# Optimization experiments

Measured on AMD Instinct MI355X. Metric: run time of the kernel, lower is better.

Reference implementation:

```python
import jax, jax.numpy as jnp
import numpy as np

EPS = 1e-12  # F.normalize eps
ALPHA = 1.0


def setup_inputs() -> dict:
    key = jax.random.key(0)
    k1, k2, k3, k4 = jax.random.split(key, 4)
    n_nodes, n_edges, d_in, d_out = 50000, 800000, 128, 128
    x = jax.random.normal(k1, (n_nodes, d_in), dtype=jnp.float32)
    W1 = jax.random.normal(k2, (d_out, d_in), dtype=jnp.float32) * (1.0 / np.sqrt(d_in))
    W2 = jax.random.normal(k3, (d_out, d_in), dtype=jnp.float32) * (1.0 / np.sqrt(d_in))
    edge_index = jax.random.randint(k4, (2, n_edges), 0, n_nodes, dtype=jnp.int64)
    return {"x": x, "W1": W1, "W2": W2, "edge_index": edge_index}


def reference(x, W1, W2, edge_index):
    n_nodes = x.shape[0]
    src, dst = edge_index[0], edge_index[1]
    # h_src = fc2(x)
    h = jnp.einsum('nd,od->no', x, W2)
    # out-degree normalization: h *= (deg_out + 1)^(-1/2)
    deg = jax.ops.segment_sum(jnp.ones(src.shape[0], dtype=x.dtype), src,
                              num_segments=n_nodes)
    h = h * ((deg + 1.0) ** -0.5)[:, None]
    # L2 normalize per node (F.normalize p=2 dim=1)
    nrm = jnp.sqrt(jnp.sum(h * h, axis=1, keepdims=True))
    h = h / jnp.maximum(nrm, EPS)
    # gather along edges, scatter-max to destinations
    msg = h[src]                                   # [E, d_out]
    agg = jax.ops.segment_max(msg, dst, num_segments=n_nodes)
    agg = jnp.where(jnp.isfinite(agg), agg, 0.0)   # empty segments -> 0 (torch_scatter semantics)
    # alpha * fc1(x) + aggregated messages
    return ALPHA * jnp.einsum('nd,od->no', x, W1) + agg
```

## Files before the change

### kernel.cpp

```cpp
#include <hip/hip_runtime.h>
#include <stdint.h>

#define N_NODES 50000
#define N_EDGES 800000
#define D 128
#define CAP 64
#define LDK 136

typedef __attribute__((ext_vector_type(8))) short short8;
typedef __attribute__((ext_vector_type(4))) float f32x4;
typedef __attribute__((ext_vector_type(4))) unsigned short ush4;

__device__ __forceinline__ unsigned short f2bf(float f) {
    uint32_t u = __float_as_uint(f);
    u += 0x7FFFu + ((u >> 16) & 1u);
    return (unsigned short)(u >> 16);
}
__device__ __forceinline__ float bflo(uint32_t u) { return __uint_as_float(u << 16); }
__device__ __forceinline__ float bfhi(uint32_t u) { return __uint_as_float(u & 0xFFFF0000u); }

__global__ __launch_bounds__(512) void gemm_fused(const float* __restrict__ x,
                                                  const float* __restrict__ W1,
                                                  const float* __restrict__ W2,
                                                  float* __restrict__ out,
                                                  unsigned short* __restrict__ hbf,
                                                  int* __restrict__ cnt)
{
    __shared__ unsigned short ws[256][LDK];
    __shared__ unsigned short xs[128][LDK];

    const int t    = threadIdx.x;
    const int row0 = blockIdx.x * 128;

    {
        int ci = blockIdx.x * 512 + t;
        if (ci < N_NODES) cnt[ci] = 0;
    }

    #pragma unroll
    for (int it = 0; it < 16; ++it) {
        int idx = it * 512 + t;
        int n = idx >> 5, c4 = idx & 31;
        const float* Wp = (n < 128) ? (W1 + (size_t)n * D) : (W2 + (size_t)(n - 128) * D);
        float4 v = *(const float4*)(Wp + c4 * 4);
        ush4 p; p[0] = f2bf(v.x); p[1] = f2bf(v.y); p[2] = f2bf(v.z); p[3] = f2bf(v.w);
        *(ush4*)&ws[n][c4 * 4] = p;
    }
    #pragma unroll
    for (int it = 0; it < 8; ++it) {
        int idx = it * 512 + t;
        int r = idx >> 5, c4 = idx & 31;
        int gr = row0 + r;
        float4 v = make_float4(0.f, 0.f, 0.f, 0.f);
        if (gr < N_NODES) v = *(const float4*)(x + (size_t)gr * D + c4 * 4);
        ush4 p; p[0] = f2bf(v.x); p[1] = f2bf(v.y); p[2] = f2bf(v.z); p[3] = f2bf(v.w);
        *(ush4*)&xs[r][c4 * 4] = p;
    }
    __syncthreads();

    const int wave = t >> 6;
    const int lane = t & 63;
    const int g    = lane >> 4;
    const int ln   = lane & 15;

    short8 afrag[4];
    #pragma unroll
    for (int ks = 0; ks < 4; ++ks)
        afrag[ks] = *(const short8*)&xs[wave * 16 + ln][ks * 32 + g * 8];

    f32x4 acc1[8], acc2[8];
    #pragma unroll
    for (int ct = 0; ct < 8; ++ct) {
        f32x4 a1 = {0.f, 0.f, 0.f, 0.f}, a2 = {0.f, 0.f, 0.f, 0.f};
        #pragma unroll
        for (int ks = 0; ks < 4; ++ks) {
            short8 b1 = *(const short8*)&ws[      ct * 16 + ln][ks * 32 + g * 8];
            short8 b2 = *(const short8*)&ws[128 + ct * 16 + ln][ks * 32 + g * 8];
            a1 = __builtin_amdgcn_mfma_f32_16x16x32_bf16(afrag[ks], b1, a1, 0, 0, 0);
            a2 = __builtin_amdgcn_mfma_f32_16x16x32_bf16(afrag[ks], b2, a2, 0, 0, 0);
        }
        acc1[ct] = a1; acc2[ct] = a2;
    }

    float ss[4] = {0.f, 0.f, 0.f, 0.f};
    #pragma unroll
    for (int ct = 0; ct < 8; ++ct)
        #pragma unroll
        for (int r = 0; r < 4; ++r)
            ss[r] = fmaf(acc2[ct][r], acc2[ct][r], ss[r]);
    #pragma unroll
    for (int r = 0; r < 4; ++r)
        #pragma unroll
        for (int o = 1; o < 16; o <<= 1)
            ss[r] += __shfl_xor(ss[r], o, 64);
    float scale[4];
    #pragma unroll
    for (int r = 0; r < 4; ++r)
        scale[r] = 1.0f / fmaxf(sqrtf(ss[r]), 1e-12f);

    #pragma unroll
    for (int r = 0; r < 4; ++r) {
        int grow = row0 + wave * 16 + g * 4 + r;
        if (grow < N_NODES) {
            #pragma unroll
            for (int ct = 0; ct < 8; ++ct) {
                out[(size_t)grow * D + ct * 16 + ln] = acc1[ct][r];
                hbf[(size_t)grow * D + ct * 16 + ln] = f2bf(acc2[ct][r] * scale[r]);
            }
        }
    }
}

__global__ __launch_bounds__(256) void fill_buckets(const int* __restrict__ ei,
                                                    int* __restrict__ cnt,
                                                    int* __restrict__ bucket)
{
    int i      = blockIdx.x * 256 + threadIdx.x;
    int stride = gridDim.x * 256;
    for (int e = i; e < N_EDGES; e += stride) {
        int s = ei[e];
        int d = ei[N_EDGES + e];
        int p = atomicAdd(&cnt[d], 1);
        if (p < CAP) bucket[d * CAP + p] = s;
    }
}

__global__ __launch_bounds__(256) void gather_max(const unsigned short* __restrict__ hbf,
                                                  const int* __restrict__ cnt,
                                                  const int* __restrict__ bucket,
                                                  float* __restrict__ out)
{
    int wid  = (blockIdx.x * 256 + threadIdx.x) >> 6;
    int lane = threadIdx.x & 63;
    if (wid >= N_NODES) return;
    int deg = cnt[wid];
    deg = (deg > CAP) ? CAP : deg;
    if (deg == 0) return;

    const uint32_t* h32 = (const uint32_t*)hbf;
    int sl = (lane < deg) ? bucket[wid * CAP + lane] : 0;

    float mx = -INFINITY, my = -INFINITY;
    int j = 0;
    for (; j + 4 <= deg; j += 4) {
        int s0 = __shfl(sl, j,     64);
        int s1 = __shfl(sl, j + 1, 64);
        int s2 = __shfl(sl, j + 2, 64);
        int s3 = __shfl(sl, j + 3, 64);
        uint32_t u0 = h32[(size_t)s0 * 64 + lane];
        uint32_t u1 = h32[(size_t)s1 * 64 + lane];
        uint32_t u2 = h32[(size_t)s2 * 64 + lane];
        uint32_t u3 = h32[(size_t)s3 * 64 + lane];
        mx = fmaxf(fmaxf(mx, bflo(u0)), fmaxf(bflo(u1), fmaxf(bflo(u2), bflo(u3))));
        my = fmaxf(fmaxf(my, bfhi(u0)), fmaxf(bfhi(u1), fmaxf(bfhi(u2), bfhi(u3))));
    }
    for (; j < deg; ++j) {
        int s = __shfl(sl, j, 64);
        uint32_t u = h32[(size_t)s * 64 + lane];
        mx = fmaxf(mx, bflo(u));
        my = fmaxf(my, bfhi(u));
    }

    float2* o2 = (float2*)out;
    float2 o = o2[(size_t)wid * 64 + lane];
    o.x += mx; o.y += my;
    o2[(size_t)wid * 64 + lane] = o;
}

extern "C" void kernel_launch(void* const* d_in, const int* in_sizes, int n_in,
                              void* d_out, int out_size, void* d_ws, size_t ws_size,
                              hipStream_t stream)
{
    const float* x  = (const float*)d_in[0];
    const float* W1 = (const float*)d_in[1];
    const float* W2 = (const float*)d_in[2];
    const int*   ei = (const int*)d_in[3];
    float* out = (float*)d_out;

    char* ws = (char*)d_ws;
    unsigned short* hbf    = (unsigned short*)ws;
    int*            cnt    = (int*)(ws + (size_t)N_NODES * D * 2);
    int*            bucket = (int*)(ws + (size_t)N_NODES * D * 2 + (size_t)N_NODES * 4);

    gemm_fused<<<(N_NODES + 127) / 128, 512, 0, stream>>>(x, W1, W2, out, hbf, cnt);
    fill_buckets<<<1024, 256, 0, stream>>>(ei, cnt, bucket);
    gather_max<<<(N_NODES * 64 + 255) / 256, 256, 0, stream>>>(hbf, cnt, bucket, out);
}
```

Measured before the change: 182.7 us.

## Split bf16 conversion into its own kernel, use 16-bit buckets, unroll gather

Moves the fp32 to bf16 conversion of x and the weights out of the GEMM into a separate grid-stride kernel that also zeroes the degree counters. The GEMM then loads bf16 fragments straight from global memory instead of staging them in LDS, with 64-row blocks of 256 threads. Bucket source indices are stored as 16-bit values to halve bucket traffic, fill_buckets runs one edge per thread, and the gather loop issues 8 loads per batch instead of 4. The trade is an extra kernel launch and an extra write and read of the bf16 copy of x, in exchange for a simpler, lower-LDS GEMM and less index traffic.

```diff
diff --git a/kernel.cpp b/kernel.cpp
--- a/kernel.cpp
+++ b/kernel.cpp
@@ -5,7 +5,6 @@
 #define N_EDGES 800000
 #define D 128
 #define CAP 64
-#define LDK 136
 
 typedef __attribute__((ext_vector_type(8))) short short8;
 typedef __attribute__((ext_vector_type(4))) float f32x4;
@@ -16,57 +15,55 @@
     u += 0x7FFFu + ((u >> 16) & 1u);
     return (unsigned short)(u >> 16);
 }
-__device__ __forceinline__ float bflo(uint32_t u) { return __uint_as_float(u << 16); }
-__device__ __forceinline__ float bfhi(uint32_t u) { return __uint_as_float(u & 0xFFFF0000u); }
+__device__ __forceinline__ float bf2f(unsigned short s) {
+    return __uint_as_float(((uint32_t)s) << 16);
+}
 
-__global__ __launch_bounds__(512) void gemm_fused(const float* __restrict__ x,
-                                                  const float* __restrict__ W1,
-                                                  const float* __restrict__ W2,
-                                                  float* __restrict__ out,
-                                                  unsigned short* __restrict__ hbf,
-                                                  int* __restrict__ cnt)
+#define X_F4   1600000
+#define W_F4   4096
+__global__ __launch_bounds__(256) void convert(const float* __restrict__ x,
+                                               const float* __restrict__ W1,
+                                               const float* __restrict__ W2,
+                                               unsigned short* __restrict__ xbf,
+                                               unsigned short* __restrict__ w1bf,
+                                               unsigned short* __restrict__ w2bf,
+                                               int* __restrict__ cnt)
 {
-    __shared__ unsigned short ws[256][LDK];
-    __shared__ unsigned short xs[128][LDK];
+    int gid    = blockIdx.x * 256 + threadIdx.x;
+    int stride = gridDim.x * 256;
+    if (gid < N_NODES) cnt[gid] = 0;
+    for (int i = gid; i < X_F4 + 2 * W_F4; i += stride) {
+        float4 v; ush4* dst;
+        if (i < X_F4)            { v = ((const float4*)x )[i];
+                                   dst = (ush4*)xbf  + i; }
+        else if (i < X_F4 + W_F4){ v = ((const float4*)W1)[i - X_F4];
+                                   dst = (ush4*)w1bf + (i - X_F4); }
+        else                     { v = ((const float4*)W2)[i - X_F4 - W_F4];
+                                   dst = (ush4*)w2bf + (i - X_F4 - W_F4); }
+        ush4 p; p[0] = f2bf(v.x); p[1] = f2bf(v.y); p[2] = f2bf(v.z); p[3] = f2bf(v.w);
+        *dst = p;
+    }
+}
 
+__global__ __launch_bounds__(256) void gemm2(const unsigned short* __restrict__ xbf,
+                                             const unsigned short* __restrict__ w1bf,
+                                             const unsigned short* __restrict__ w2bf,
+                                             float* __restrict__ out,
+                                             unsigned short* __restrict__ hbf)
+{
     const int t    = threadIdx.x;
-    const int row0 = blockIdx.x * 128;
-
-    {
-        int ci = blockIdx.x * 512 + t;
-        if (ci < N_NODES) cnt[ci] = 0;
-    }
-
-    #pragma unroll
-    for (int it = 0; it < 16; ++it) {
-        int idx = it * 512 + t;
-        int n = idx >> 5, c4 = idx & 31;
-        const float* Wp = (n < 128) ? (W1 + (size_t)n * D) : (W2 + (size_t)(n - 128) * D);
-        float4 v = *(const float4*)(Wp + c4 * 4);
-        ush4 p; p[0] = f2bf(v.x); p[1] = f2bf(v.y); p[2] = f2bf(v.z); p[3] = f2bf(v.w);
-        *(ush4*)&ws[n][c4 * 4] = p;
-    }
-    #pragma unroll
-    for (int it = 0; it < 8; ++it) {
-        int idx = it * 512 + t;
-        int r = idx >> 5, c4 = idx & 31;
-        int gr = row0 + r;
-        float4 v = make_float4(0.f, 0.f, 0.f, 0.f);
-        if (gr < N_NODES) v = *(const float4*)(x + (size_t)gr * D + c4 * 4);
-        ush4 p; p[0] = f2bf(v.x); p[1] = f2bf(v.y); p[2] = f2bf(v.z); p[3] = f2bf(v.w);
-        *(ush4*)&xs[r][c4 * 4] = p;
-    }
-    __syncthreads();
-
     const int wave = t >> 6;
     const int lane = t & 63;
     const int g    = lane >> 4;
     const int ln   = lane & 15;
+    const int rowbase = blockIdx.x * 64 + wave * 16;
 
+    int arow = rowbase + ln;
+    int arowc = (arow < N_NODES) ? arow : (N_NODES - 1);
     short8 afrag[4];
     #pragma unroll
     for (int ks = 0; ks < 4; ++ks)
-        afrag[ks] = *(const short8*)&xs[wave * 16 + ln][ks * 32 + g * 8];
+        afrag[ks] = *(const short8*)&xbf[(size_t)arowc * D + ks * 32 + g * 8];
 
     f32x4 acc1[8], acc2[8];
     #pragma unroll
@@ -74,8 +71,8 @@
         f32x4 a1 = {0.f, 0.f, 0.f, 0.f}, a2 = {0.f, 0.f, 0.f, 0.f};
         #pragma unroll
         for (int ks = 0; ks < 4; ++ks) {
-            short8 b1 = *(const short8*)&ws[      ct * 16 + ln][ks * 32 + g * 8];
-            short8 b2 = *(const short8*)&ws[128 + ct * 16 + ln][ks * 32 + g * 8];
+            short8 b1 = *(const short8*)&w1bf[(ct * 16 + ln) * D + ks * 32 + g * 8];
+            short8 b2 = *(const short8*)&w2bf[(ct * 16 + ln) * D + ks * 32 + g * 8];
             a1 = __builtin_amdgcn_mfma_f32_16x16x32_bf16(afrag[ks], b1, a1, 0, 0, 0);
             a2 = __builtin_amdgcn_mfma_f32_16x16x32_bf16(afrag[ks], b2, a2, 0, 0, 0);
         }
@@ -100,7 +97,7 @@
 
     #pragma unroll
     for (int r = 0; r < 4; ++r) {
-        int grow = row0 + wave * 16 + g * 4 + r;
+        int grow = rowbase + g * 4 + r;
         if (grow < N_NODES) {
             #pragma unroll
             for (int ct = 0; ct < 8; ++ct) {
@@ -113,21 +110,19 @@
 
 __global__ __launch_bounds__(256) void fill_buckets(const int* __restrict__ ei,
                                                     int* __restrict__ cnt,
-                                                    int* __restrict__ bucket)
+                                                    unsigned short* __restrict__ bucket)
 {
-    int i      = blockIdx.x * 256 + threadIdx.x;
-    int stride = gridDim.x * 256;
-    for (int e = i; e < N_EDGES; e += stride) {
-        int s = ei[e];
-        int d = ei[N_EDGES + e];
-        int p = atomicAdd(&cnt[d], 1);
-        if (p < CAP) bucket[d * CAP + p] = s;
-    }
+    int e = blockIdx.x * 256 + threadIdx.x;
+    if (e >= N_EDGES) return;
+    int s = ei[e];
+    int d = ei[N_EDGES + e];
+    int p = atomicAdd(&cnt[d], 1);
+    if (p < CAP) bucket[d * CAP + p] = (unsigned short)s;
 }
 
 __global__ __launch_bounds__(256) void gather_max(const unsigned short* __restrict__ hbf,
                                                   const int* __restrict__ cnt,
-                                                  const int* __restrict__ bucket,
+                                                  const unsigned short* __restrict__ bucket,
                                                   float* __restrict__ out)
 {
     int wid  = (blockIdx.x * 256 + threadIdx.x) >> 6;
@@ -138,27 +133,28 @@
     if (deg == 0) return;
 
     const uint32_t* h32 = (const uint32_t*)hbf;
-    int sl = (lane < deg) ? bucket[wid * CAP + lane] : 0;
+    int sl = (lane < deg) ? (int)bucket[wid * CAP + lane] : 0;
 
     float mx = -INFINITY, my = -INFINITY;
     int j = 0;
-    for (; j + 4 <= deg; j += 4) {
-        int s0 = __shfl(sl, j,     64);
-        int s1 = __shfl(sl, j + 1, 64);
-        int s2 = __shfl(sl, j + 2, 64);
-        int s3 = __shfl(sl, j + 3, 64);
-        uint32_t u0 = h32[(size_t)s0 * 64 + lane];
-        uint32_t u1 = h32[(size_t)s1 * 64 + lane];
-        uint32_t u2 = h32[(size_t)s2 * 64 + lane];
-        uint32_t u3 = h32[(size_t)s3 * 64 + lane];
-        mx = fmaxf(fmaxf(mx, bflo(u0)), fmaxf(bflo(u1), fmaxf(bflo(u2), bflo(u3))));
-        my = fmaxf(fmaxf(my, bfhi(u0)), fmaxf(bfhi(u1), fmaxf(bfhi(u2), bfhi(u3))));
+    for (; j + 8 <= deg; j += 8) {
+        uint32_t u[8];
+        #pragma unroll
+        for (int q = 0; q < 8; ++q) {
+            int s = __shfl(sl, j + q, 64);
+            u[q] = h32[(size_t)s * 64 + lane];
+        }
+        #pragma unroll
+        for (int q = 0; q < 8; ++q) {
+            mx = fmaxf(mx, __uint_as_float(u[q] << 16));
+            my = fmaxf(my, __uint_as_float(u[q] & 0xFFFF0000u));
+        }
     }
     for (; j < deg; ++j) {
         int s = __shfl(sl, j, 64);
         uint32_t u = h32[(size_t)s * 64 + lane];
-        mx = fmaxf(mx, bflo(u));
-        my = fmaxf(my, bfhi(u));
+        mx = fmaxf(mx, __uint_as_float(u << 16));
+        my = fmaxf(my, __uint_as_float(u & 0xFFFF0000u));
     }
 
     float2* o2 = (float2*)out;
@@ -178,11 +174,16 @@
     float* out = (float*)d_out;
 
     char* ws = (char*)d_ws;
-    unsigned short* hbf    = (unsigned short*)ws;
-    int*            cnt    = (int*)(ws + (size_t)N_NODES * D * 2);
-    int*            bucket = (int*)(ws + (size_t)N_NODES * D * 2 + (size_t)N_NODES * 4);
+    const size_t XBF = (size_t)N_NODES * D * 2;
+    unsigned short* xbf    = (unsigned short*)ws;
+    unsigned short* hbf    = (unsigned short*)(ws + XBF);
+    unsigned short* w1bf   = (unsigned short*)(ws + 2 * XBF);
+    unsigned short* w2bf   = (unsigned short*)(ws + 2 * XBF + 32768);
+    int*            cnt    = (int*)(ws + 2 * XBF + 65536);
+    unsigned short* bucket = (unsigned short*)(ws + 2 * XBF + 65536 + 200704);
 
-    gemm_fused<<<(N_NODES + 127) / 128, 512, 0, stream>>>(x, W1, W2, out, hbf, cnt);
-    fill_buckets<<<1024, 256, 0, stream>>>(ei, cnt, bucket);
+    convert<<<2048, 256, 0, stream>>>(x, W1, W2, xbf, w1bf, w2bf, cnt);
+    gemm2<<<(N_NODES + 63) / 64, 256, 0, stream>>>(xbf, w1bf, w2bf, out, hbf);
+    fill_buckets<<<(N_EDGES + 255) / 256, 256, 0, stream>>>(ei, cnt, bucket);
     gather_max<<<(N_NODES * 64 + 255) / 256, 256, 0, stream>>>(hbf, cnt, bucket, out);
 }
```

Result: slower. 200.8 us (+9.9%).

## Fuse edge bucketing into GEMM kernel, store 16-bit bucket indices, unroll gather

Applied to the files above, without the earlier changes.

Edge bucketing now runs inside the GEMM kernel: each thread loads four edges up front, issues its atomic counter increments after the shared-memory staging, and writes bucket entries after the GEMM epilogue. The aim is to hide atomic and edge-load latency behind the matrix work and remove a separate kernel launch. The counter array is now zeroed by a hipMemsetAsync, because another block could otherwise increment a counter before the block that owns it clears it. Source indices are stored as 16-bit values, which works only because the node count is below 65536. The gather loop is unrolled to eight loads in flight per step.

```diff
diff --git a/kernel.cpp b/kernel.cpp
--- a/kernel.cpp
+++ b/kernel.cpp
@@ -6,6 +6,8 @@
 #define D 128
 #define CAP 64
 #define LDK 136
+#define NBLK 391
+#define NT_FILL (NBLK * 512)
 
 typedef __attribute__((ext_vector_type(8))) short short8;
 typedef __attribute__((ext_vector_type(4))) float f32x4;
@@ -16,25 +18,30 @@
     u += 0x7FFFu + ((u >> 16) & 1u);
     return (unsigned short)(u >> 16);
 }
-__device__ __forceinline__ float bflo(uint32_t u) { return __uint_as_float(u << 16); }
-__device__ __forceinline__ float bfhi(uint32_t u) { return __uint_as_float(u & 0xFFFF0000u); }
 
-__global__ __launch_bounds__(512) void gemm_fused(const float* __restrict__ x,
-                                                  const float* __restrict__ W1,
-                                                  const float* __restrict__ W2,
-                                                  float* __restrict__ out,
-                                                  unsigned short* __restrict__ hbf,
-                                                  int* __restrict__ cnt)
+__global__ __launch_bounds__(512) void gemm_fill(const float* __restrict__ x,
+                                                 const float* __restrict__ W1,
+                                                 const float* __restrict__ W2,
+                                                 const int* __restrict__ ei,
+                                                 float* __restrict__ out,
+                                                 unsigned short* __restrict__ hbf,
+                                                 int* __restrict__ cnt,
+                                                 unsigned short* __restrict__ bucket)
 {
-    __shared__ unsigned short ws[256][LDK];
+    __shared__ unsigned short wsm[256][LDK];
     __shared__ unsigned short xs[128][LDK];
 
     const int t    = threadIdx.x;
     const int row0 = blockIdx.x * 128;
+    const int gid  = blockIdx.x * 512 + t;
 
-    {
-        int ci = blockIdx.x * 512 + t;
-        if (ci < N_NODES) cnt[ci] = 0;
+    int es[4], ed[4];
+    #pragma unroll
+    for (int k = 0; k < 4; ++k) {
+        int e = gid + k * NT_FILL;
+        bool v = (e < N_EDGES);
+        es[k] = v ? ei[e] : 0;
+        ed[k] = v ? ei[N_EDGES + e] : -1;
     }
 
     #pragma unroll
@@ -44,7 +51,7 @@
         const float* Wp = (n < 128) ? (W1 + (size_t)n * D) : (W2 + (size_t)(n - 128) * D);
         float4 v = *(const float4*)(Wp + c4 * 4);
         ush4 p; p[0] = f2bf(v.x); p[1] = f2bf(v.y); p[2] = f2bf(v.z); p[3] = f2bf(v.w);
-        *(ush4*)&ws[n][c4 * 4] = p;
+        *(ush4*)&wsm[n][c4 * 4] = p;
     }
     #pragma unroll
     for (int it = 0; it < 8; ++it) {
@@ -57,6 +64,11 @@
         *(ush4*)&xs[r][c4 * 4] = p;
     }
     __syncthreads();
+
+    int ep[4];
+    #pragma unroll
+    for (int k = 0; k < 4; ++k)
+        ep[k] = (ed[k] >= 0) ? atomicAdd(&cnt[ed[k]], 1) : CAP;
 
     const int wave = t >> 6;
     const int lane = t & 63;
@@ -74,8 +86,8 @@
         f32x4 a1 = {0.f, 0.f, 0.f, 0.f}, a2 = {0.f, 0.f, 0.f, 0.f};
         #pragma unroll
         for (int ks = 0; ks < 4; ++ks) {
-            short8 b1 = *(const short8*)&ws[      ct * 16 + ln][ks * 32 + g * 8];
-            short8 b2 = *(const short8*)&ws[128 + ct * 16 + ln][ks * 32 + g * 8];
+            short8 b1 = *(const short8*)&wsm[      ct * 16 + ln][ks * 32 + g * 8];
+            short8 b2 = *(const short8*)&wsm[128 + ct * 16 + ln][ks * 32 + g * 8];
             a1 = __builtin_amdgcn_mfma_f32_16x16x32_bf16(afrag[ks], b1, a1, 0, 0, 0);
             a2 = __builtin_amdgcn_mfma_f32_16x16x32_bf16(afrag[ks], b2, a2, 0, 0, 0);
         }
@@ -109,25 +121,16 @@
             }
         }
     }
-}
 
-__global__ __launch_bounds__(256) void fill_buckets(const int* __restrict__ ei,
-                                                    int* __restrict__ cnt,
-                                                    int* __restrict__ bucket)
-{
-    int i      = blockIdx.x * 256 + threadIdx.x;
-    int stride = gridDim.x * 256;
-    for (int e = i; e < N_EDGES; e += stride) {
-        int s = ei[e];
-        int d = ei[N_EDGES + e];
-        int p = atomicAdd(&cnt[d], 1);
-        if (p < CAP) bucket[d * CAP + p] = s;
-    }
+    #pragma unroll
+    for (int k = 0; k < 4; ++k)
+        if (ed[k] >= 0 && ep[k] < CAP)
+            bucket[ed[k] * CAP + ep[k]] = (unsigned short)es[k];
 }
 
 __global__ __launch_bounds__(256) void gather_max(const unsigned short* __restrict__ hbf,
                                                   const int* __restrict__ cnt,
-                                                  const int* __restrict__ bucket,
+                                                  const unsigned short* __restrict__ bucket,
                                                   float* __restrict__ out)
 {
     int wid  = (blockIdx.x * 256 + threadIdx.x) >> 6;
@@ -138,27 +141,28 @@
     if (deg == 0) return;
 
     const uint32_t* h32 = (const uint32_t*)hbf;
-    int sl = (lane < deg) ? bucket[wid * CAP + lane] : 0;
+    int sl = (lane < deg) ? (int)bucket[wid * CAP + lane] : 0;
 
     float mx = -INFINITY, my = -INFINITY;
     int j = 0;
-    for (; j + 4 <= deg; j += 4) {
-        int s0 = __shfl(sl, j,     64);
-        int s1 = __shfl(sl, j + 1, 64);
-        int s2 = __shfl(sl, j + 2, 64);
-        int s3 = __shfl(sl, j + 3, 64);
-        uint32_t u0 = h32[(size_t)s0 * 64 + lane];
-        uint32_t u1 = h32[(size_t)s1 * 64 + lane];
-        uint32_t u2 = h32[(size_t)s2 * 64 + lane];
-        uint32_t u3 = h32[(size_t)s3 * 64 + lane];
-        mx = fmaxf(fmaxf(mx, bflo(u0)), fmaxf(bflo(u1), fmaxf(bflo(u2), bflo(u3))));
-        my = fmaxf(fmaxf(my, bfhi(u0)), fmaxf(bfhi(u1), fmaxf(bfhi(u2), bfhi(u3))));
+    for (; j + 8 <= deg; j += 8) {
+        uint32_t u[8];
+        #pragma unroll
+        for (int q = 0; q < 8; ++q) {
+            int s = __shfl(sl, j + q, 64);
+            u[q] = h32[(size_t)s * 64 + lane];
+        }
+        #pragma unroll
+        for (int q = 0; q < 8; ++q) {
+            mx = fmaxf(mx, __uint_as_float(u[q] << 16));
+            my = fmaxf(my, __uint_as_float(u[q] & 0xFFFF0000u));
+        }
     }
     for (; j < deg; ++j) {
         int s = __shfl(sl, j, 64);
         uint32_t u = h32[(size_t)s * 64 + lane];
-        mx = fmaxf(mx, bflo(u));
-        my = fmaxf(my, bfhi(u));
+        mx = fmaxf(mx, __uint_as_float(u << 16));
+        my = fmaxf(my, __uint_as_float(u & 0xFFFF0000u));
     }
 
     float2* o2 = (float2*)out;
@@ -180,9 +184,10 @@
     char* ws = (char*)d_ws;
     unsigned short* hbf    = (unsigned short*)ws;
     int*            cnt    = (int*)(ws + (size_t)N_NODES * D * 2);
-    int*            bucket = (int*)(ws + (size_t)N_NODES * D * 2 + (size_t)N_NODES * 4);
+    unsigned short* bucket = (unsigned short*)(ws + (size_t)N_NODES * D * 2
+                                                  + (size_t)N_NODES * 4);
 
-    gemm_fused<<<(N_NODES + 127) / 128, 512, 0, stream>>>(x, W1, W2, out, hbf, cnt);
-    fill_buckets<<<1024, 256, 0, stream>>>(ei, cnt, bucket);
+    hipMemsetAsync(cnt, 0, (size_t)N_NODES * 4, stream);
+    gemm_fill<<<NBLK, 512, 0, stream>>>(x, W1, W2, ei, out, hbf, cnt, bucket);
     gather_max<<<(N_NODES * 64 + 255) / 256, 256, 0, stream>>>(hbf, cnt, bucket, out);
 }
```

New measurement: 162.2 us. 1.13x faster.
